# Performance work log

Measured on AMD Instinct MI355X. Metric: run time of the kernel, lower is better.

The kernel has to match this reference:

```python
import jax, jax.numpy as jnp
import numpy as np

B, S, H, A = 32, 4096, 512, 256

def setup_inputs() -> dict:
    key = jax.random.key(0)
    ks = jax.random.split(key, 8)
    sH = 1.0 / np.sqrt(H)
    sA = 1.0 / np.sqrt(A)
    return {
        "encoder_outputs": jax.random.normal(ks[0], (B, S, H), dtype=jnp.float32),
        "decoder_hidden": jax.random.normal(ks[1], (B, H), dtype=jnp.float32),
        "W_enc": jax.random.uniform(ks[2], (H, A), jnp.float32, -sH, sH),
        "b_enc": jax.random.uniform(ks[3], (A,), jnp.float32, -sH, sH),
        "W_dec": jax.random.uniform(ks[4], (H, A), jnp.float32, -sH, sH),
        "b_dec": jax.random.uniform(ks[5], (A,), jnp.float32, -sH, sH),
        "W_e": jax.random.uniform(ks[6], (A,), jnp.float32, -sA, sA),
        "b_e": jax.random.uniform(ks[7], (), jnp.float32, -sA, sA),
    }

def reference(encoder_outputs, decoder_hidden, W_enc, b_enc, W_dec, b_dec, W_e, b_e):
    # [B,S,A] encoder projection
    enc_p = jnp.einsum('bsh,ha->bsa', encoder_outputs, W_enc) + b_enc
    # [B,1,A] decoder projection broadcast over S
    dec_p = (decoder_hidden @ W_dec + b_dec)[:, None, :]
    scores = jnp.einsum('bsa,a->bs', jnp.tanh(enc_p + dec_p), W_e) + b_e  # [B,S]
    attn = jax.nn.softmax(scores, axis=1)                                 # [B,S]
    context = jnp.einsum('bs,bsh->bh', attn, encoder_outputs)             # [B,H]
    return context, attn
```

## Files before the change

### kernel.cpp

```cpp
#include <hip/hip_runtime.h>
#include <hip/hip_bf16.h>
#include <stdint.h>


typedef __attribute__((ext_vector_type(4))) float f32x4;
typedef __attribute__((ext_vector_type(8))) short short8;

#define B_  32
#define S_  4096
#define H_  512
#define A_  256

#define WS_WT     0
#define WS_BIAS   262144
#define WS_SCORES 294912
#define WS_PART   819200

static __device__ __forceinline__ short f2bf(float f) {
  union { float f; uint32_t u; } v; v.f = f;
  uint32_t r = (v.u + 0x7FFFu + ((v.u >> 16) & 1u)) >> 16;
  return (short)(uint16_t)r;
}

static __device__ __forceinline__ void gload_lds16(const void* g, void* l) {
  __builtin_amdgcn_global_load_lds((const __attribute__((address_space(1))) void*)g,
                                   (__attribute__((address_space(3))) void*)l,
                                   16, 0, 0);
}

__global__ void prep_kernel(const float* __restrict__ dh,
                            const float* __restrict__ W_enc,
                            const float* __restrict__ b_enc,
                            const float* __restrict__ W_dec,
                            const float* __restrict__ b_dec,
                            unsigned short* __restrict__ WT,
                            float* __restrict__ bias) {
  int tid = threadIdx.x;
  if (blockIdx.x < 32) {
    int b = blockIdx.x;
    float s = b_enc[tid] + b_dec[tid];
    const float* dhb = dh + (size_t)b * H_;
    #pragma unroll 8
    for (int k = 0; k < H_; ++k)
      s = fmaf(dhb[k], W_dec[(size_t)k * A_ + tid], s);
    bias[b * A_ + tid] = s;
  } else {
    int t = (blockIdx.x - 32) * 256 + tid;
    #pragma unroll
    for (int i = 0; i < 16; ++i) {
      int idx = t + i * 8192;
      int k = idx >> 8, n = idx & 255;
      WT[(size_t)n * H_ + k] = (unsigned short)f2bf(W_enc[idx]);
    }
  }
}

__global__ __launch_bounds__(256, 2) void scores_gemm(
    const float* __restrict__ enc,
    const unsigned short* __restrict__ WT,
    const float* __restrict__ bias,
    const float* __restrict__ We,
    float* __restrict__ scores) {
  __shared__ __align__(16) unsigned short Bt[256 * 32];

  const int tid  = threadIdx.x;
  const int wave = tid >> 6, lane = tid & 63;
  const int lm   = lane & 15, lq = lane >> 4;
  const int row0 = blockIdx.x * 128;
  const int b    = blockIdx.x >> 5;

  f32x4 acc[2][16];
  #pragma unroll
  for (int mt = 0; mt < 2; ++mt)
    #pragma unroll
    for (int nt = 0; nt < 16; ++nt)
      acc[mt][nt] = (f32x4){0.f, 0.f, 0.f, 0.f};

  size_t aoff[2];
  #pragma unroll
  for (int mt = 0; mt < 2; ++mt)
    aoff[mt] = (size_t)(row0 + wave * 32 + mt * 16 + lm) * H_ + lq * 8;

  float4 ca[2][2];
  #pragma unroll
  for (int mt = 0; mt < 2; ++mt) {
    const float* ap = enc + aoff[mt];
    ca[mt][0] = *(const float4*)ap;
    ca[mt][1] = *(const float4*)(ap + 4);
  }

  const int bn = (wave * 4) * 16 + (lane >> 2);
  const int kb = (lane & 3) * 8;

  for (int k0 = 0; k0 < H_; k0 += 32) {
    __syncthreads();
    #pragma unroll
    for (int c = 0; c < 4; ++c) {
      int n = bn + c * 16;
      gload_lds16(WT + (size_t)n * H_ + k0 + kb,
                  (char*)Bt + (size_t)(wave * 4 + c) * 1024);
    }
    float4 na[2][2];
    const int kn = k0 + 32;
    if (kn < H_) {
      #pragma unroll
      for (int mt = 0; mt < 2; ++mt) {
        const float* ap = enc + aoff[mt] + kn;
        na[mt][0] = *(const float4*)ap;
        na[mt][1] = *(const float4*)(ap + 4);
      }
    }
    __syncthreads();

    short8 af[2];
    #pragma unroll
    for (int mt = 0; mt < 2; ++mt) {
      af[mt][0] = f2bf(ca[mt][0].x); af[mt][1] = f2bf(ca[mt][0].y);
      af[mt][2] = f2bf(ca[mt][0].z); af[mt][3] = f2bf(ca[mt][0].w);
      af[mt][4] = f2bf(ca[mt][1].x); af[mt][5] = f2bf(ca[mt][1].y);
      af[mt][6] = f2bf(ca[mt][1].z); af[mt][7] = f2bf(ca[mt][1].w);
    }
    #pragma unroll
    for (int nt = 0; nt < 16; ++nt) {
      short8 bf = *(const short8*)((const char*)Bt + (size_t)(nt * 16 + lm) * 64 + lq * 16);
      #pragma unroll
      for (int mt = 0; mt < 2; ++mt)
        acc[mt][nt] = __builtin_amdgcn_mfma_f32_16x16x32_bf16(af[mt], bf, acc[mt][nt], 0, 0, 0);
    }
    if (kn < H_) {
      #pragma unroll
      for (int mt = 0; mt < 2; ++mt) { ca[mt][0] = na[mt][0]; ca[mt][1] = na[mt][1]; }
    }
  }

  float psum[2][4] = {{0, 0, 0, 0}, {0, 0, 0, 0}};
  #pragma unroll
  for (int nt = 0; nt < 16; ++nt) {
    int col = nt * 16 + lm;
    float dp = bias[b * A_ + col];
    float wv = We[col];
    #pragma unroll
    for (int mt = 0; mt < 2; ++mt)
      #pragma unroll
      for (int r = 0; r < 4; ++r) {
        float x = acc[mt][nt][r] + dp;
        float e = __expf(2.0f * x);
        float t = 1.0f - 2.0f * __builtin_amdgcn_rcpf(e + 1.0f);
        psum[mt][r] = fmaf(t, wv, psum[mt][r]);
      }
  }
  #pragma unroll
  for (int o = 1; o < 16; o <<= 1)
    #pragma unroll
    for (int mt = 0; mt < 2; ++mt)
      #pragma unroll
      for (int r = 0; r < 4; ++r)
        psum[mt][r] += __shfl_xor(psum[mt][r], o, 64);
  if (lm == 0) {
    #pragma unroll
    for (int mt = 0; mt < 2; ++mt)
      #pragma unroll
      for (int r = 0; r < 4; ++r)
        scores[row0 + wave * 32 + mt * 16 + lq * 4 + r] = psum[mt][r];
  }
}

__global__ void softmax_kernel(const float* __restrict__ scores,
                               float* __restrict__ attn) {
  int b = blockIdx.x, tid = threadIdx.x;
  int wave = tid >> 6, lane = tid & 63;
  const float4* sp = (const float4*)(scores + (size_t)b * S_);
  float4 v[4];
  #pragma unroll
  for (int i = 0; i < 4; ++i) v[i] = sp[tid + i * 256];

  float m = -1e30f;
  #pragma unroll
  for (int i = 0; i < 4; ++i) {
    m = fmaxf(m, fmaxf(fmaxf(v[i].x, v[i].y), fmaxf(v[i].z, v[i].w)));
  }
  #pragma unroll
  for (int o = 1; o < 64; o <<= 1) m = fmaxf(m, __shfl_xor(m, o, 64));
  __shared__ float redm[4];
  if (lane == 0) redm[wave] = m;
  __syncthreads();
  m = fmaxf(fmaxf(redm[0], redm[1]), fmaxf(redm[2], redm[3]));

  float sum = 0.f;
  float4 p[4];
  #pragma unroll
  for (int i = 0; i < 4; ++i) {
    p[i].x = __expf(v[i].x - m); p[i].y = __expf(v[i].y - m);
    p[i].z = __expf(v[i].z - m); p[i].w = __expf(v[i].w - m);
    sum += p[i].x + p[i].y + p[i].z + p[i].w;
  }
  #pragma unroll
  for (int o = 1; o < 64; o <<= 1) sum += __shfl_xor(sum, o, 64);
  __shared__ float reds[4];
  if (lane == 0) reds[wave] = sum;
  __syncthreads();
  float inv = 1.0f / (reds[0] + reds[1] + reds[2] + reds[3]);

  float4* op = (float4*)(attn + (size_t)b * S_);
  #pragma unroll
  for (int i = 0; i < 4; ++i) {
    float4 o4; o4.x = p[i].x * inv; o4.y = p[i].y * inv;
    o4.z = p[i].z * inv; o4.w = p[i].w * inv;
    op[tid + i * 256] = o4;
  }
}

__global__ void ctx_partial(const float* __restrict__ enc,
                            const float* __restrict__ attn,
                            float* __restrict__ part) {
  int b = blockIdx.x >> 5, c = blockIdx.x & 31;
  int tid = threadIdx.x;
  __shared__ float aw[128];
  if (tid < 128) aw[tid] = attn[(size_t)b * S_ + c * 128 + tid];
  __syncthreads();
  const float* ebase = enc + ((size_t)b * S_ + c * 128) * H_ + tid * 2;
  float sx = 0.f, sy = 0.f;
  #pragma unroll 4
  for (int i = 0; i < 128; ++i) {
    float2 e = *(const float2*)(ebase + (size_t)i * H_);
    float a = aw[i];
    sx = fmaf(a, e.x, sx); sy = fmaf(a, e.y, sy);
  }
  float2 o; o.x = sx; o.y = sy;
  *(float2*)(part + ((size_t)(b * 32 + c)) * H_ + tid * 2) = o;
}

__global__ void ctx_reduce(const float* __restrict__ part,
                           float* __restrict__ ctx) {
  int b = blockIdx.x, tid = threadIdx.x;
  float sx = 0.f, sy = 0.f;
  #pragma unroll
  for (int c = 0; c < 32; ++c) {
    float2 p = *(const float2*)(part + ((size_t)(b * 32 + c)) * H_ + tid * 2);
    sx += p.x; sy += p.y;
  }
  float2 o; o.x = sx; o.y = sy;
  *(float2*)(ctx + (size_t)b * H_ + tid * 2) = o;
}

extern "C" void kernel_launch(void* const* d_in, const int* in_sizes, int n_in,
                              void* d_out, int out_size, void* d_ws, size_t ws_size,
                              hipStream_t stream) {
  const float* enc   = (const float*)d_in[0];
  const float* dh    = (const float*)d_in[1];
  const float* W_enc = (const float*)d_in[2];
  const float* b_enc = (const float*)d_in[3];
  const float* W_dec = (const float*)d_in[4];
  const float* b_dec = (const float*)d_in[5];
  const float* W_e   = (const float*)d_in[6];

  char* ws = (char*)d_ws;
  unsigned short* WT = (unsigned short*)(ws + WS_WT);
  float* bias   = (float*)(ws + WS_BIAS);
  float* scores = (float*)(ws + WS_SCORES);
  float* part   = (float*)(ws + WS_PART);

  float* ctx  = (float*)d_out;
  float* attn = (float*)d_out + B_ * H_;

  prep_kernel<<<dim3(64), dim3(256), 0, stream>>>(dh, W_enc, b_enc, W_dec, b_dec, WT, bias);
  scores_gemm<<<dim3(1024), dim3(256), 0, stream>>>(enc, WT, bias, W_e, scores);
  softmax_kernel<<<dim3(32), dim3(256), 0, stream>>>(scores, attn);
  ctx_partial<<<dim3(1024), dim3(256), 0, stream>>>(enc, attn, part);
  ctx_reduce<<<dim3(32), dim3(256), 0, stream>>>(part, ctx);
}
```

Measured before the change: 454.5 us.

## Fuse score GEMM, chunked online softmax and context into one pass over encoder

Scores, a per-chunk softmax (local max and sum) and the partial context are computed in one kernel. The bf16 encoder tile is kept in LDS so encoder_outputs is read from HBM only once instead of twice. A finalize kernel rescales the chunk partials with the global max and sum to produce the context and attention outputs. The W^T operand is now read straight from global memory rather than staged in LDS, the context is built from bf16-rounded encoder values (a precision risk), and prep uses an LDS-tiled transpose.

```diff
diff --git a/kernel.cpp b/kernel.cpp
--- a/kernel.cpp
+++ b/kernel.cpp
@@ -14,233 +14,197 @@
 #define WS_WT     0
 #define WS_BIAS   262144
 #define WS_SCORES 294912
-#define WS_PART   819200
+#define WS_M      819200
+#define WS_L      827392
+#define WS_PART   835584
 
 static __device__ __forceinline__ short f2bf(float f) {
   union { float f; uint32_t u; } v; v.f = f;
   uint32_t r = (v.u + 0x7FFFu + ((v.u >> 16) & 1u)) >> 16;
   return (short)(uint16_t)r;
 }
-
-static __device__ __forceinline__ void gload_lds16(const void* g, void* l) {
-  __builtin_amdgcn_global_load_lds((const __attribute__((address_space(1))) void*)g,
-                                   (__attribute__((address_space(3))) void*)l,
-                                   16, 0, 0);
-}
-
-__global__ void prep_kernel(const float* __restrict__ dh,
-                            const float* __restrict__ W_enc,
-                            const float* __restrict__ b_enc,
-                            const float* __restrict__ W_dec,
-                            const float* __restrict__ b_dec,
-                            unsigned short* __restrict__ WT,
-                            float* __restrict__ bias) {
-  int tid = threadIdx.x;
+static __device__ __forceinline__ float bf2f(uint32_t lo16) {
+  union { uint32_t u; float f; } v; v.u = lo16 << 16; return v.f;
+}
+
+__global__ __launch_bounds__(256) void prep_kernel(
+    const float* __restrict__ dh, const float* __restrict__ W_enc,
+    const float* __restrict__ b_enc, const float* __restrict__ W_dec,
+    const float* __restrict__ b_dec, unsigned short* __restrict__ WT,
+    float* __restrict__ bias) {
+  __shared__ float dh_s[512];
+  __shared__ unsigned short tile[64 * 66];
+  const int tid = threadIdx.x;
   if (blockIdx.x < 32) {
-    int b = blockIdx.x;
-    float s = b_enc[tid] + b_dec[tid];
-    const float* dhb = dh + (size_t)b * H_;
+    const int b = blockIdx.x;
+    dh_s[tid]       = dh[(size_t)b * H_ + tid];
+    dh_s[tid + 256] = dh[(size_t)b * H_ + tid + 256];
+    __syncthreads();
+    float s[4] = {0.f, 0.f, 0.f, 0.f};
+    for (int k = 0; k < H_; k += 32) {
+      #pragma unroll
+      for (int j = 0; j < 32; ++j)
+        s[j & 3] = fmaf(dh_s[k + j], W_dec[(size_t)(k + j) * A_ + tid], s[j & 3]);
+    }
+    bias[b * A_ + tid] = s[0] + s[1] + s[2] + s[3] + b_enc[tid] + b_dec[tid];
+  } else {
+    const int t = blockIdx.x - 32;
+    const int kt = t >> 2, nt2 = t & 3;
+    #pragma unroll
+    for (int i = 0; i < 16; ++i) {
+      int idx = tid + i * 256;
+      int kk = idx >> 6, nn = idx & 63;
+      tile[kk * 66 + nn] =
+          (unsigned short)f2bf(W_enc[(size_t)(kt * 64 + kk) * A_ + nt2 * 64 + nn]);
+    }
+    __syncthreads();
+    #pragma unroll
+    for (int i = 0; i < 16; ++i) {
+      int idx = tid + i * 256;
+      int nn = idx >> 6, kk = idx & 63;
+      WT[(size_t)(nt2 * 64 + nn) * H_ + kt * 64 + kk] = tile[kk * 66 + nn];
+    }
+  }
+}
+
+__global__ __launch_bounds__(256, 2) void fused_kernel(
+    const float* __restrict__ enc, const unsigned short* __restrict__ WT,
+    const float* __restrict__ bias, const float* __restrict__ We,
+    float* __restrict__ scores, float* __restrict__ wsm,
+    float* __restrict__ wsl, float* __restrict__ part) {
+  __shared__ __align__(16) unsigned short A_lds[64 * 520];
+  __shared__ float s_sc[64];
+  __shared__ float s_e[64];
+  __shared__ float s_ml[2];
+
+  const int tid = threadIdx.x, w = tid >> 6, lane = tid & 63;
+  const int lm = lane & 15, lq = lane >> 4;
+  const int b = blockIdx.x >> 6;
+  const int chunk = blockIdx.x & 63;
+  const int srow0 = blockIdx.x * 64;
+  const int arow_l = w * 16 + lm;
+
+  f32x4 acc[16];
+  #pragma unroll
+  for (int nt = 0; nt < 16; ++nt) acc[nt] = (f32x4){0.f, 0.f, 0.f, 0.f};
+
+  const float* ap = enc + (size_t)(srow0 + arow_l) * H_ + lq * 8;
+  const unsigned short* wtp = WT + (size_t)lm * H_ + lq * 8;
+
+  float4 ca0 = *(const float4*)ap;
+  float4 ca1 = *(const float4*)(ap + 4);
+  for (int k0 = 0; k0 < H_; k0 += 32) {
+    float4 na0, na1;
+    const int kn = k0 + 32;
+    if (kn < H_) { na0 = *(const float4*)(ap + kn); na1 = *(const float4*)(ap + kn + 4); }
+    short8 af;
+    af[0] = f2bf(ca0.x); af[1] = f2bf(ca0.y); af[2] = f2bf(ca0.z); af[3] = f2bf(ca0.w);
+    af[4] = f2bf(ca1.x); af[5] = f2bf(ca1.y); af[6] = f2bf(ca1.z); af[7] = f2bf(ca1.w);
+    *(short8*)&A_lds[arow_l * 520 + k0 + lq * 8] = af;
+    #pragma unroll
+    for (int nt = 0; nt < 16; ++nt) {
+      short8 bf = *(const short8*)(wtp + (size_t)nt * 16 * H_ + k0);
+      acc[nt] = __builtin_amdgcn_mfma_f32_16x16x32_bf16(af, bf, acc[nt], 0, 0, 0);
+    }
+    if (kn < H_) { ca0 = na0; ca1 = na1; }
+  }
+
+  float psum[4] = {0.f, 0.f, 0.f, 0.f};
+  #pragma unroll
+  for (int nt = 0; nt < 16; ++nt) {
+    const int col = nt * 16 + lm;
+    const float dp = bias[b * A_ + col];
+    const float wv = We[col];
+    #pragma unroll
+    for (int r = 0; r < 4; ++r) {
+      float x = acc[nt][r] + dp;
+      float e = __expf(2.0f * x);
+      float t = 1.0f - 2.0f * __builtin_amdgcn_rcpf(e + 1.0f);
+      psum[r] = fmaf(t, wv, psum[r]);
+    }
+  }
+  #pragma unroll
+  for (int o = 1; o < 16; o <<= 1)
+    #pragma unroll
+    for (int r = 0; r < 4; ++r)
+      psum[r] += __shfl_xor(psum[r], o, 64);
+  if (lm == 0) {
+    #pragma unroll
+    for (int r = 0; r < 4; ++r) {
+      const int rl = w * 16 + lq * 4 + r;
+      s_sc[rl] = psum[r];
+      scores[srow0 + rl] = psum[r];
+    }
+  }
+  __syncthreads();
+
+  if (tid < 64) {
+    float sc = s_sc[tid];
+    float m = sc;
+    #pragma unroll
+    for (int o = 1; o < 64; o <<= 1) m = fmaxf(m, __shfl_xor(m, o, 64));
+    float e = __expf(sc - m);
+    float l = e;
+    #pragma unroll
+    for (int o = 1; o < 64; o <<= 1) l += __shfl_xor(l, o, 64);
+    s_e[tid] = e;
+    if (tid == 0) {
+      wsm[b * 64 + chunk] = m;
+      wsl[b * 64 + chunk] = l;
+    }
+  }
+  __syncthreads();
+
+  float cx0 = 0.f, cx1 = 0.f;
+  #pragma unroll 8
+  for (int row = 0; row < 64; ++row) {
+    uint32_t pv = *(const uint32_t*)&A_lds[row * 520 + (tid << 1)];
+    float wr = s_e[row];
+    cx0 = fmaf(wr, bf2f(pv & 0xffffu), cx0);
+    cx1 = fmaf(wr, bf2f(pv >> 16), cx1);
+  }
+  float2 o2; o2.x = cx0; o2.y = cx1;
+  *(float2*)&part[(size_t)(b * 64 + chunk) * H_ + (tid << 1)] = o2;
+}
+
+__global__ __launch_bounds__(256) void finalize_kernel(
+    const float* __restrict__ scores, const float* __restrict__ wsm,
+    const float* __restrict__ wsl, const float* __restrict__ part,
+    float* __restrict__ ctx, float* __restrict__ attn) {
+  __shared__ float wgt[64];
+  __shared__ float s_ml[2];
+  const int b = blockIdx.x, tid = threadIdx.x;
+  if (tid < 64) {
+    float mc = wsm[b * 64 + tid];
+    float lc = wsl[b * 64 + tid];
+    float M = mc;
+    #pragma unroll
+    for (int o = 1; o < 64; o <<= 1) M = fmaxf(M, __shfl_xor(M, o, 64));
+    float wv = __expf(mc - M);
+    float Lp = wv * lc;
+    #pragma unroll
+    for (int o = 1; o < 64; o <<= 1) Lp += __shfl_xor(Lp, o, 64);
+    wgt[tid] = wv;
+    if (tid == 0) { s_ml[0] = M; s_ml[1] = Lp; }
+  }
+  __syncthreads();
+  const float M = s_ml[0];
+  const float invL = 1.0f / s_ml[1];
+
+  #pragma unroll
+  for (int hh = 0; hh < 2; ++hh) {
+    const int h = tid + hh * 256;
+    float s = 0.f;
     #pragma unroll 8
-    for (int k = 0; k < H_; ++k)
-      s = fmaf(dhb[k], W_dec[(size_t)k * A_ + tid], s);
-    bias[b * A_ + tid] = s;
-  } else {
-    int t = (blockIdx.x - 32) * 256 + tid;
-    #pragma unroll
-    for (int i = 0; i < 16; ++i) {
-      int idx = t + i * 8192;
-      int k = idx >> 8, n = idx & 255;
-      WT[(size_t)n * H_ + k] = (unsigned short)f2bf(W_enc[idx]);
-    }
-  }
-}
-
-__global__ __launch_bounds__(256, 2) void scores_gemm(
-    const float* __restrict__ enc,
-    const unsigned short* __restrict__ WT,
-    const float* __restrict__ bias,
-    const float* __restrict__ We,
-    float* __restrict__ scores) {
-  __shared__ __align__(16) unsigned short Bt[256 * 32];
-
-  const int tid  = threadIdx.x;
-  const int wave = tid >> 6, lane = tid & 63;
-  const int lm   = lane & 15, lq = lane >> 4;
-  const int row0 = blockIdx.x * 128;
-  const int b    = blockIdx.x >> 5;
-
-  f32x4 acc[2][16];
-  #pragma unroll
-  for (int mt = 0; mt < 2; ++mt)
-    #pragma unroll
-    for (int nt = 0; nt < 16; ++nt)
-      acc[mt][nt] = (f32x4){0.f, 0.f, 0.f, 0.f};
-
-  size_t aoff[2];
-  #pragma unroll
-  for (int mt = 0; mt < 2; ++mt)
-    aoff[mt] = (size_t)(row0 + wave * 32 + mt * 16 + lm) * H_ + lq * 8;
-
-  float4 ca[2][2];
-  #pragma unroll
-  for (int mt = 0; mt < 2; ++mt) {
-    const float* ap = enc + aoff[mt];
-    ca[mt][0] = *(const float4*)ap;
-    ca[mt][1] = *(const float4*)(ap + 4);
-  }
-
-  const int bn = (wave * 4) * 16 + (lane >> 2);
-  const int kb = (lane & 3) * 8;
-
-  for (int k0 = 0; k0 < H_; k0 += 32) {
-    __syncthreads();
-    #pragma unroll
-    for (int c = 0; c < 4; ++c) {
-      int n = bn + c * 16;
-      gload_lds16(WT + (size_t)n * H_ + k0 + kb,
-                  (char*)Bt + (size_t)(wave * 4 + c) * 1024);
-    }
-    float4 na[2][2];
-    const int kn = k0 + 32;
-    if (kn < H_) {
-      #pragma unroll
-      for (int mt = 0; mt < 2; ++mt) {
-        const float* ap = enc + aoff[mt] + kn;
-        na[mt][0] = *(const float4*)ap;
-        na[mt][1] = *(const float4*)(ap + 4);
-      }
-    }
-    __syncthreads();
-
-    short8 af[2];
-    #pragma unroll
-    for (int mt = 0; mt < 2; ++mt) {
-      af[mt][0] = f2bf(ca[mt][0].x); af[mt][1] = f2bf(ca[mt][0].y);
-      af[mt][2] = f2bf(ca[mt][0].z); af[mt][3] = f2bf(ca[mt][0].w);
-      af[mt][4] = f2bf(ca[mt][1].x); af[mt][5] = f2bf(ca[mt][1].y);
-      af[mt][6] = f2bf(ca[mt][1].z); af[mt][7] = f2bf(ca[mt][1].w);
-    }
-    #pragma unroll
-    for (int nt = 0; nt < 16; ++nt) {
-      short8 bf = *(const short8*)((const char*)Bt + (size_t)(nt * 16 + lm) * 64 + lq * 16);
-      #pragma unroll
-      for (int mt = 0; mt < 2; ++mt)
-        acc[mt][nt] = __builtin_amdgcn_mfma_f32_16x16x32_bf16(af[mt], bf, acc[mt][nt], 0, 0, 0);
-    }
-    if (kn < H_) {
-      #pragma unroll
-      for (int mt = 0; mt < 2; ++mt) { ca[mt][0] = na[mt][0]; ca[mt][1] = na[mt][1]; }
-    }
-  }
-
-  float psum[2][4] = {{0, 0, 0, 0}, {0, 0, 0, 0}};
-  #pragma unroll
-  for (int nt = 0; nt < 16; ++nt) {
-    int col = nt * 16 + lm;
-    float dp = bias[b * A_ + col];
-    float wv = We[col];
-    #pragma unroll
-    for (int mt = 0; mt < 2; ++mt)
-      #pragma unroll
-      for (int r = 0; r < 4; ++r) {
-        float x = acc[mt][nt][r] + dp;
-        float e = __expf(2.0f * x);
-        float t = 1.0f - 2.0f * __builtin_amdgcn_rcpf(e + 1.0f);
-        psum[mt][r] = fmaf(t, wv, psum[mt][r]);
-      }
-  }
-  #pragma unroll
-  for (int o = 1; o < 16; o <<= 1)
-    #pragma unroll
-    for (int mt = 0; mt < 2; ++mt)
-      #pragma unroll
-      for (int r = 0; r < 4; ++r)
-        psum[mt][r] += __shfl_xor(psum[mt][r], o, 64);
-  if (lm == 0) {
-    #pragma unroll
-    for (int mt = 0; mt < 2; ++mt)
-      #pragma unroll
-      for (int r = 0; r < 4; ++r)
-        scores[row0 + wave * 32 + mt * 16 + lq * 4 + r] = psum[mt][r];
-  }
-}
-
-__global__ void softmax_kernel(const float* __restrict__ scores,
-                               float* __restrict__ attn) {
-  int b = blockIdx.x, tid = threadIdx.x;
-  int wave = tid >> 6, lane = tid & 63;
-  const float4* sp = (const float4*)(scores + (size_t)b * S_);
-  float4 v[4];
-  #pragma unroll
-  for (int i = 0; i < 4; ++i) v[i] = sp[tid + i * 256];
-
-  float m = -1e30f;
-  #pragma unroll
-  for (int i = 0; i < 4; ++i) {
-    m = fmaxf(m, fmaxf(fmaxf(v[i].x, v[i].y), fmaxf(v[i].z, v[i].w)));
-  }
-  #pragma unroll
-  for (int o = 1; o < 64; o <<= 1) m = fmaxf(m, __shfl_xor(m, o, 64));
-  __shared__ float redm[4];
-  if (lane == 0) redm[wave] = m;
-  __syncthreads();
-  m = fmaxf(fmaxf(redm[0], redm[1]), fmaxf(redm[2], redm[3]));
-
-  float sum = 0.f;
-  float4 p[4];
-  #pragma unroll
-  for (int i = 0; i < 4; ++i) {
-    p[i].x = __expf(v[i].x - m); p[i].y = __expf(v[i].y - m);
-    p[i].z = __expf(v[i].z - m); p[i].w = __expf(v[i].w - m);
-    sum += p[i].x + p[i].y + p[i].z + p[i].w;
-  }
-  #pragma unroll
-  for (int o = 1; o < 64; o <<= 1) sum += __shfl_xor(sum, o, 64);
-  __shared__ float reds[4];
-  if (lane == 0) reds[wave] = sum;
-  __syncthreads();
-  float inv = 1.0f / (reds[0] + reds[1] + reds[2] + reds[3]);
-
-  float4* op = (float4*)(attn + (size_t)b * S_);
-  #pragma unroll
-  for (int i = 0; i < 4; ++i) {
-    float4 o4; o4.x = p[i].x * inv; o4.y = p[i].y * inv;
-    o4.z = p[i].z * inv; o4.w = p[i].w * inv;
-    op[tid + i * 256] = o4;
-  }
-}
-
-__global__ void ctx_partial(const float* __restrict__ enc,
-                            const float* __restrict__ attn,
-                            float* __restrict__ part) {
-  int b = blockIdx.x >> 5, c = blockIdx.x & 31;
-  int tid = threadIdx.x;
-  __shared__ float aw[128];
-  if (tid < 128) aw[tid] = attn[(size_t)b * S_ + c * 128 + tid];
-  __syncthreads();
-  const float* ebase = enc + ((size_t)b * S_ + c * 128) * H_ + tid * 2;
-  float sx = 0.f, sy = 0.f;
-  #pragma unroll 4
-  for (int i = 0; i < 128; ++i) {
-    float2 e = *(const float2*)(ebase + (size_t)i * H_);
-    float a = aw[i];
-    sx = fmaf(a, e.x, sx); sy = fmaf(a, e.y, sy);
-  }
-  float2 o; o.x = sx; o.y = sy;
-  *(float2*)(part + ((size_t)(b * 32 + c)) * H_ + tid * 2) = o;
-}
-
-__global__ void ctx_reduce(const float* __restrict__ part,
-                           float* __restrict__ ctx) {
-  int b = blockIdx.x, tid = threadIdx.x;
-  float sx = 0.f, sy = 0.f;
-  #pragma unroll
-  for (int c = 0; c < 32; ++c) {
-    float2 p = *(const float2*)(part + ((size_t)(b * 32 + c)) * H_ + tid * 2);
-    sx += p.x; sy += p.y;
-  }
-  float2 o; o.x = sx; o.y = sy;
-  *(float2*)(ctx + (size_t)b * H_ + tid * 2) = o;
+    for (int c = 0; c < 64; ++c)
+      s = fmaf(wgt[c], part[(size_t)(b * 64 + c) * H_ + h], s);
+    ctx[(size_t)b * H_ + h] = s * invL;
+  }
+  #pragma unroll
+  for (int i = 0; i < 16; ++i) {
+    const int s_ = tid + i * 256;
+    attn[(size_t)b * S_ + s_] = __expf(scores[(size_t)b * S_ + s_] - M) * invL;
+  }
 }
 
 extern "C" void kernel_launch(void* const* d_in, const int* in_sizes, int n_in,
@@ -258,14 +222,14 @@
   unsigned short* WT = (unsigned short*)(ws + WS_WT);
   float* bias   = (float*)(ws + WS_BIAS);
   float* scores = (float*)(ws + WS_SCORES);
+  float* wsm    = (float*)(ws + WS_M);
+  float* wsl    = (float*)(ws + WS_L);
   float* part   = (float*)(ws + WS_PART);
 
   float* ctx  = (float*)d_out;
   float* attn = (float*)d_out + B_ * H_;
 
   prep_kernel<<<dim3(64), dim3(256), 0, stream>>>(dh, W_enc, b_enc, W_dec, b_dec, WT, bias);
-  scores_gemm<<<dim3(1024), dim3(256), 0, stream>>>(enc, WT, bias, W_e, scores);
-  softmax_kernel<<<dim3(32), dim3(256), 0, stream>>>(scores, attn);
-  ctx_partial<<<dim3(1024), dim3(256), 0, stream>>>(enc, attn, part);
-  ctx_reduce<<<dim3(32), dim3(256), 0, stream>>>(part, ctx);
-}
+  fused_kernel<<<dim3(2048), dim3(256), 0, stream>>>(enc, WT, bias, W_e, scores, wsm, wsl, part);
+  finalize_kernel<<<dim3(32), dim3(256), 0, stream>>>(scores, wsm, wsl, part, ctx, attn);
+}
```

Result: slower. 587.3 us (+29.2%).
